# Kernel tuning notes

Hardware: AMD Instinct MI355X
Metric: run time of the kernel (lower is better)

The kernel has to match this reference:

```python
import jax, jax.numpy as jnp
import numpy as np

B, L, E, H, V = 64, 128, 512, 512, 32000  # batch, output_length, emb_dim, hidden, vocab


def setup_inputs() -> dict:
    key = jax.random.key(0)
    ks = jax.random.split(key, 9)
    g = lambda k, shape, sc=0.02: jax.random.normal(k, shape, jnp.float32) * sc
    return {
        "decoder_inputs": jax.random.randint(ks[0], (B, L), 0, V),
        "hidden": jax.random.normal(ks[1], (1, B, H), jnp.float32),  # size-only; zeroed in forward
        "encoder_outputs": jax.random.normal(ks[2], (B, L, H), jnp.float32),
        "emb_table": g(ks[3], (V, E)),
        "W_attn": g(ks[4], (L, 2 * H)),
        "b_attn": jnp.zeros((L,), jnp.float32),
        "W_ih": g(ks[5], (3 * H, E)),
        "W_hh": g(ks[6], (3 * H, H)),
        "b_ih": jnp.zeros((3 * H,), jnp.float32),
        "b_hh": jnp.zeros((3 * H,), jnp.float32),
        "W_out": g(ks[7], (V, H)),
        "b_out": jnp.zeros((V,), jnp.float32),
    }


def reference(decoder_inputs, hidden, encoder_outputs, emb_table, W_attn, b_attn,
              W_ih, W_hh, b_ih, b_hh, W_out, b_out):
    # teacher_force=True, train=True path; dropout = identity (eval semantics).
    T = L - 1  # output_length - 1 steps
    embedded = emb_table[decoder_inputs]                      # [B, L, E]
    h0 = jnp.zeros((B, H), embedded.dtype)                    # init_hidden(): hidden is zeroed
    # decode_input at step i is embedded[:, max(i-1, 0)] under teacher forcing
    prev_idx = jnp.maximum(jnp.arange(T) - 1, 0)
    dec_in_seq = jnp.transpose(embedded[:, prev_idx], (1, 0, 2))  # [T, B, E]
    x_seq = jnp.transpose(embedded[:, :T], (1, 0, 2))             # [T, B, E] GRU inputs
    tgt_seq = decoder_inputs[:, :T].T                             # [T, B]

    def step(carry, xs):
        h, loss = carry
        dec_in, x, tgt = xs
        attn_logits = jnp.concatenate([dec_in, h], axis=-1) @ W_attn.T + b_attn  # [B, L]
        aw = jax.nn.softmax(attn_logits, axis=-1)
        _ = jnp.einsum('bl,blh->bh', aw, encoder_outputs)  # attn_applied (computed, unused w/ teacher forcing)
        # single-step GRU cell (PyTorch gate order: r, z, n)
        gi = x @ W_ih.T + b_ih                                # [B, 3H]
        gh = h @ W_hh.T + b_hh
        ir, iz, inn = jnp.split(gi, 3, axis=-1)
        hr, hz, hn = jnp.split(gh, 3, axis=-1)
        r = jax.nn.sigmoid(ir + hr)
        z = jax.nn.sigmoid(iz + hz)
        n = jnp.tanh(inn + r * hn)
        h_new = (1.0 - z) * n + z * h
        logits = h_new @ W_out.T + b_out                      # [B, V]
        logp = jax.nn.log_softmax(logits, axis=-1)
        ce = -jnp.take_along_axis(logp, tgt[:, None], axis=1).mean()
        return (h_new, loss + ce), (aw, logits)

    (h_fin, loss), (attns, logits_all) = jax.lax.scan(
        step, (h0, jnp.asarray(0.0, jnp.float32)), (dec_in_seq, x_seq, tgt_seq))
    return loss, attns, h_fin[None], logits_all[-1]
```

## Files before the change

### kernel.cpp

```cpp
#include <hip/hip_runtime.h>
#include <math.h>

#define Bn 64
#define Lq 128
#define En 512
#define Hn 512
#define Vn 32000
#define Tn 127
#define MR 8128
#define MP 8192
#define NCB2 250
#define NBLK 36u

typedef __attribute__((ext_vector_type(8))) short short8v;
typedef __attribute__((ext_vector_type(4))) float f32x4;
typedef unsigned short ushort_t;

__device__ __forceinline__ ushort_t f2bf(float f) {
    unsigned u = __builtin_bit_cast(unsigned, f);
    u += 0x7fffu + ((u >> 16) & 1u);
    return (ushort_t)(u >> 16);
}
__device__ __forceinline__ float bf2f(ushort_t h) {
    return __builtin_bit_cast(float, ((unsigned)h) << 16);
}

constexpr size_t WS_BAR  = 0;
constexpr size_t WS_ZBH  = 64;
constexpr size_t WS_ZBL  = WS_ZBH + 65536;
constexpr size_t WS_WHHH = WS_ZBL + 65536;
constexpr size_t WS_WHHL = WS_WHHH + 1572864;
constexpr size_t WS_WAHH = WS_WHHL + 1572864;
constexpr size_t WS_WAHL = WS_WAHH + 131072;
constexpr size_t WS_HHI  = WS_WAHL + 131072;
constexpr size_t WS_HLO  = WS_HHI + 8388608;
constexpr size_t WS_U    = WS_HLO + 8388608;
constexpr size_t WS_GI   = WS_U;
constexpr size_t WS_GAX  = WS_U + 49938432;
constexpr size_t WS_WO16 = WS_U;
constexpr size_t WS_PM   = WS_U + 32768000;
constexpr size_t WS_PS   = WS_PM + 8192000;

__device__ __forceinline__ void grid_bar(unsigned* bar, unsigned tgt) {
    __syncthreads();
    if (threadIdx.x == 0) {
        __hip_atomic_fetch_add(bar, 1u, __ATOMIC_ACQ_REL, __HIP_MEMORY_SCOPE_AGENT);
        while (__hip_atomic_load(bar, __ATOMIC_RELAXED, __HIP_MEMORY_SCOPE_AGENT) < tgt) { }
        (void)__hip_atomic_load(bar, __ATOMIC_ACQUIRE, __HIP_MEMORY_SCOPE_AGENT);
    }
    __syncthreads();
}

__global__ __launch_bounds__(256) void setup_kernel(
    const float* __restrict__ Whh, const float* __restrict__ Wattn,
    ushort_t* __restrict__ zbh, ushort_t* __restrict__ zbl,
    ushort_t* __restrict__ whhh, ushort_t* __restrict__ whhl,
    ushort_t* __restrict__ wahh, ushort_t* __restrict__ wahl,
    ushort_t* __restrict__ Hhi, ushort_t* __restrict__ Hlo,
    unsigned* __restrict__ bar, float* __restrict__ out0)
{
    const int blk = blockIdx.x;
    const int t = threadIdx.x;
    if (blk < 256) {
        const int i = blk * 256 + t;
        if (i < Bn * Hn) { zbh[i] = 0; zbl[i] = 0; }
        else if (i < 2 * Bn * Hn) {
            const int j = i - Bn * Hn;
            Hhi[(size_t)MR * Hn + j] = 0;
            Hlo[(size_t)MR * Hn + j] = 0;
        }
        if (i == 0) { bar[0] = 0u; out0[0] = 0.0f; }
    } else {
        const int e = (blk - 256) * 256 + t;
        const int NW = 1536 * 512;
        if (e < NW) {
            const float wv = Whh[e]; const ushort_t h = f2bf(wv);
            whhh[e] = h; whhl[e] = f2bf(wv - bf2f(h));
        } else {
            const int e2 = e - NW;
            if (e2 < 128 * 512) {
                const int r = e2 >> 9, k = e2 & 511;
                const float wv = Wattn[r * 1024 + 512 + k]; const ushort_t h = f2bf(wv);
                wahh[e2] = h; wahl[e2] = f2bf(wv - bf2f(h));
            }
        }
    }
}

__global__ __launch_bounds__(256) void wout_cvt_kernel(
    const float* __restrict__ Wout, ushort_t* __restrict__ wo16)
{
    const size_t N = (size_t)Vn * Hn;
    for (size_t i = blockIdx.x * 256 + threadIdx.x; i < N; i += (size_t)gridDim.x * 256)
        wo16[i] = f2bf(Wout[i]);
}

#define PA 68
#define PW 132
__device__ void pre_tile(
    const int* __restrict__ idx, const float* __restrict__ emb,
    const float* __restrict__ Wb, int ldw, const float* __restrict__ bias,
    float* __restrict__ outp, int ldo, int ts, int cbase,
    float* As, float* Ws)
{
    const int t  = threadIdx.x;
    const int tr = t >> 4, tc = t & 15;

    float acc[4][8];
    #pragma unroll
    for (int q = 0; q < 4; q++)
        #pragma unroll
        for (int j = 0; j < 8; j++) acc[q][j] = 0.0f;

    const int ab = t & 63, kq = t >> 6;
    const int wc = t >> 1, wh = t & 1;

    for (int k0 = 0; k0 < 512; k0 += 32) {
        {
            const float* ap = emb + (size_t)idx[ab * Lq + ts] * En + k0 + kq * 8;
            const float4 v0 = *reinterpret_cast<const float4*>(ap);
            const float4 v1 = *reinterpret_cast<const float4*>(ap + 4);
            const int kk = kq * 8;
            As[(kk + 0) * PA + ab] = v0.x;  As[(kk + 1) * PA + ab] = v0.y;
            As[(kk + 2) * PA + ab] = v0.z;  As[(kk + 3) * PA + ab] = v0.w;
            As[(kk + 4) * PA + ab] = v1.x;  As[(kk + 5) * PA + ab] = v1.y;
            As[(kk + 6) * PA + ab] = v1.z;  As[(kk + 7) * PA + ab] = v1.w;
        }
        {
            const float* wp = Wb + (size_t)(cbase + wc) * ldw + k0 + wh * 16;
            const float4 w0 = reinterpret_cast<const float4*>(wp)[0];
            const float4 w1 = reinterpret_cast<const float4*>(wp)[1];
            const float4 w2 = reinterpret_cast<const float4*>(wp)[2];
            const float4 w3 = reinterpret_cast<const float4*>(wp)[3];
            const int kk = wh * 16;
            Ws[(kk + 0 ) * PW + wc] = w0.x; Ws[(kk + 1 ) * PW + wc] = w0.y;
            Ws[(kk + 2 ) * PW + wc] = w0.z; Ws[(kk + 3 ) * PW + wc] = w0.w;
            Ws[(kk + 4 ) * PW + wc] = w1.x; Ws[(kk + 5 ) * PW + wc] = w1.y;
            Ws[(kk + 6 ) * PW + wc] = w1.z; Ws[(kk + 7 ) * PW + wc] = w1.w;
            Ws[(kk + 8 ) * PW + wc] = w2.x; Ws[(kk + 9 ) * PW + wc] = w2.y;
            Ws[(kk + 10) * PW + wc] = w2.z; Ws[(kk + 11) * PW + wc] = w2.w;
            Ws[(kk + 12) * PW + wc] = w3.x; Ws[(kk + 13) * PW + wc] = w3.y;
            Ws[(kk + 14) * PW + wc] = w3.z; Ws[(kk + 15) * PW + wc] = w3.w;
        }
        __syncthreads();
        #pragma unroll 4
        for (int kk = 0; kk < 32; kk++) {
            const float4 av = *reinterpret_cast<const float4*>(&As[kk * PA + tr * 4]);
            const float4 w0 = *reinterpret_cast<const float4*>(&Ws[kk * PW + tc * 8]);
            const float4 w1 = *reinterpret_cast<const float4*>(&Ws[kk * PW + tc * 8 + 4]);
            const float a0 = av.x, a1 = av.y, a2 = av.z, a3 = av.w;
            const float w[8] = {w0.x, w0.y, w0.z, w0.w, w1.x, w1.y, w1.z, w1.w};
            #pragma unroll
            for (int j = 0; j < 8; j++) {
                acc[0][j] = fmaf(a0, w[j], acc[0][j]);
                acc[1][j] = fmaf(a1, w[j], acc[1][j]);
                acc[2][j] = fmaf(a2, w[j], acc[2][j]);
                acc[3][j] = fmaf(a3, w[j], acc[3][j]);
            }
        }
        __syncthreads();
    }

    #pragma unroll
    for (int q = 0; q < 4; q++) {
        const int row = tr * 4 + q;
        #pragma unroll
        for (int j = 0; j < 8; j++) {
            const int lc = tc * 8 + j;
            outp[((size_t)ts * 64 + row) * ldo + cbase + lc] = acc[q][j] + bias[cbase + lc];
        }
    }
}

__global__ __launch_bounds__(256) void pre_all_kernel(
    const int* __restrict__ idx, const float* __restrict__ emb,
    const float* __restrict__ Wih, const float* __restrict__ bih,
    const float* __restrict__ Wattn, const float* __restrict__ battn,
    float* __restrict__ Gi, float* __restrict__ Gax)
{
    __shared__ float As[32 * PA];
    __shared__ float Ws[32 * PW];
    const int blk = blockIdx.x;
    if (blk < Tn * 12) {
        pre_tile(idx, emb, Wih, 512, bih, Gi, 1536, blk / 12, (blk % 12) * 128, As, Ws);
    } else {
        pre_tile(idx, emb, Wattn, 1024, battn, Gax, 128, blk - Tn * 12, 0, As, Ws);
    }
}

__global__ __launch_bounds__(256) void recur_kernel(
    const ushort_t* __restrict__ zbh, const ushort_t* __restrict__ zbl,
    const ushort_t* __restrict__ whhh, const ushort_t* __restrict__ whhl,
    const ushort_t* __restrict__ wahh, const ushort_t* __restrict__ wahl,
    const float* __restrict__ Gi, const float* __restrict__ Gax,
    const float* __restrict__ b_hh,
    ushort_t* __restrict__ Hhi, ushort_t* __restrict__ Hlo,
    float* __restrict__ out_attn, float* __restrict__ out_hfin,
    unsigned* __restrict__ bar)
{
    __shared__ float lS[16][128];
    const int blk = blockIdx.x;
    const int t = threadIdx.x;
    const int w = t >> 6, l = t & 63, lr = l & 15, lg = l >> 4;

    if (blk < 32) {
        const int r0 = (blk >> 3) * 16;
        const int u0 = (blk & 7) * 64;
        const int c  = u0 + w * 16 + lr;
        const ushort_t* bh0 = whhh + (size_t)(c)        * Hn + lg * 8;
        const ushort_t* bh1 = whhh + (size_t)(512 + c)  * Hn + lg * 8;
        const ushort_t* bh2 = whhh + (size_t)(1024 + c) * Hn + lg * 8;
        const ushort_t* bl0 = whhl + (size_t)(c)        * Hn + lg * 8;
        const ushort_t* bl1 = whhl + (size_t)(512 + c)  * Hn + lg * 8;
        const ushort_t* bl2 = whhl + (size_t)(1024 + c) * Hn + lg * 8;
        const float bhr = b_hh[c], bhz = b_hh[512 + c], bhn = b_hh[1024 + c];

        for (int s = 0; s < Tn; s++) {
            const ushort_t* hh = (s == 0) ? zbh : (Hhi + (size_t)(s - 1) * (Bn * Hn));
            const ushort_t* hl = (s == 0) ? zbl : (Hlo + (size_t)(s - 1) * (Bn * Hn));
            const ushort_t* ah = hh + (size_t)(r0 + lr) * Hn + lg * 8;
            const ushort_t* al = hl + (size_t)(r0 + lr) * Hn + lg * 8;

            f32x4 a0 = {0.f,0.f,0.f,0.f}, a1 = {0.f,0.f,0.f,0.f}, a2 = {0.f,0.f,0.f,0.f};
            #pragma unroll 2
            for (int ks = 0; ks < 16; ks++) {
                const int k0 = ks * 32;
                const short8v xh  = *reinterpret_cast<const short8v*>(ah + k0);
                const short8v xlo = *reinterpret_cast<const short8v*>(al + k0);
                const short8v w0h = *reinterpret_cast<const short8v*>(bh0 + k0);
                const short8v w1h = *reinterpret_cast<const short8v*>(bh1 + k0);
                const short8v w2h = *reinterpret_cast<const short8v*>(bh2 + k0);
                const short8v w0l = *reinterpret_cast<const short8v*>(bl0 + k0);
                const short8v w1l = *reinterpret_cast<const short8v*>(bl1 + k0);
                const short8v w2l = *reinterpret_cast<const short8v*>(bl2 + k0);
                a0 = __builtin_amdgcn_mfma_f32_16x16x32_bf16(xh,  w0h, a0, 0, 0, 0);
                a0 = __builtin_amdgcn_mfma_f32_16x16x32_bf16(xlo, w0h, a0, 0, 0, 0);
                a0 = __builtin_amdgcn_mfma_f32_16x16x32_bf16(xh,  w0l, a0, 0, 0, 0);
                a1 = __builtin_amdgcn_mfma_f32_16x16x32_bf16(xh,  w1h, a1, 0, 0, 0);
                a1 = __builtin_amdgcn_mfma_f32_16x16x32_bf16(xlo, w1h, a1, 0, 0, 0);
                a1 = __builtin_amdgcn_mfma_f32_16x16x32_bf16(xh,  w1l, a1, 0, 0, 0);
                a2 = __builtin_amdgcn_mfma_f32_16x16x32_bf16(xh,  w2h, a2, 0, 0, 0);
                a2 = __builtin_amdgcn_mfma_f32_16x16x32_bf16(xlo, w2h, a2, 0, 0, 0);
                a2 = __builtin_amdgcn_mfma_f32_16x16x32_bf16(xh,  w2l, a2, 0, 0, 0);
            }
            #pragma unroll
            for (int i = 0; i < 4; i++) {
                const int grow = r0 + lg * 4 + i;
                const float* gib = Gi + ((size_t)s * Bn + grow) * 1536 + c;
                const float gir = gib[0], giz = gib[512], gin = gib[1024];
                const float ghr = a0[i] + bhr, ghz = a1[i] + bhz, ghn = a2[i] + bhn;
                const float rr = 1.0f / (1.0f + expf(-(gir + ghr)));
                const float zz = 1.0f / (1.0f + expf(-(giz + ghz)));
                const float nn = tanhf(gin + rr * ghn);
                const float ho = bf2f(hh[(size_t)grow * Hn + c]) + bf2f(hl[(size_t)grow * Hn + c]);
                const float hv = (1.0f - zz) * nn + zz * ho;
                const ushort_t hi = f2bf(hv);
                const size_t o = ((size_t)s * Bn + grow) * Hn + c;
                Hhi[o] = hi;
                Hlo[o] = f2bf(hv - bf2f(hi));
                if (s == Tn - 1) out_hfin[(size_t)grow * Hn + c] = hv;
            }
            if (s < Tn - 1) grid_bar(bar, NBLK * (unsigned)(s + 1));
        }
    } else {
        const int r0 = (blk - 32) * 16;
        const ushort_t* bh0 = wahh + (size_t)(w * 32 + lr)      * Hn + lg * 8;
        const ushort_t* bh1 = wahh + (size_t)(w * 32 + 16 + lr) * Hn + lg * 8;
        const ushort_t* bl0 = wahl + (size_t)(w * 32 + lr)      * Hn + lg * 8;
        const ushort_t* bl1 = wahl + (size_t)(w * 32 + 16 + lr) * Hn + lg * 8;

        for (int s = 0; s < Tn; s++) {
            const ushort_t* hh = (s == 0) ? zbh : (Hhi + (size_t)(s - 1) * (Bn * Hn));
            const ushort_t* hl = (s == 0) ? zbl : (Hlo + (size_t)(s - 1) * (Bn * Hn));
            const ushort_t* ah = hh + (size_t)(r0 + lr) * Hn + lg * 8;
            const ushort_t* al = hl + (size_t)(r0 + lr) * Hn + lg * 8;

            f32x4 c0a = {0.f,0.f,0.f,0.f}, c1a = {0.f,0.f,0.f,0.f};
            #pragma unroll 2
            for (int ks = 0; ks < 16; ks++) {
                const int k0 = ks * 32;
                const short8v xh  = *reinterpret_cast<const short8v*>(ah + k0);
                const short8v xlo = *reinterpret_cast<const short8v*>(al + k0);
                const short8v w0h = *reinterpret_cast<const short8v*>(bh0 + k0);
                const short8v w1h = *reinterpret_cast<const short8v*>(bh1 + k0);
                const short8v w0l = *reinterpret_cast<const short8v*>(bl0 + k0);
                const short8v w1l = *reinterpret_cast<const short8v*>(bl1 + k0);
                c0a = __builtin_amdgcn_mfma_f32_16x16x32_bf16(xh,  w0h, c0a, 0, 0, 0);
                c0a = __builtin_amdgcn_mfma_f32_16x16x32_bf16(xlo, w0h, c0a, 0, 0, 0);
                c0a = __builtin_amdgcn_mfma_f32_16x16x32_bf16(xh,  w0l, c0a, 0, 0, 0);
                c1a = __builtin_amdgcn_mfma_f32_16x16x32_bf16(xh,  w1h, c1a, 0, 0, 0);
                c1a = __builtin_amdgcn_mfma_f32_16x16x32_bf16(xlo, w1h, c1a, 0, 0, 0);
                c1a = __builtin_amdgcn_mfma_f32_16x16x32_bf16(xh,  w1l, c1a, 0, 0, 0);
            }
            const int jp = (s > 0) ? (s - 1) : 0;
            #pragma unroll
            for (int i = 0; i < 4; i++) {
                const int row = lg * 4 + i;
                const float* gax = Gax + ((size_t)jp * Bn + r0 + row) * Lq;
                lS[row][w * 32 + lr]      = c0a[i] + gax[w * 32 + lr];
                lS[row][w * 32 + 16 + lr] = c1a[i] + gax[w * 32 + 16 + lr];
            }
            __syncthreads();
            {
                const int row = t >> 4, l16 = t & 15;
                float m = -INFINITY;
                #pragma unroll
                for (int kx = 0; kx < 8; kx++) m = fmaxf(m, lS[row][l16 + kx * 16]);
                #pragma unroll
                for (int d = 1; d < 16; d <<= 1) m = fmaxf(m, __shfl_xor(m, d, 16));
                float sv = 0.0f;
                #pragma unroll
                for (int kx = 0; kx < 8; kx++) sv += expf(lS[row][l16 + kx * 16] - m);
                #pragma unroll
                for (int d = 1; d < 16; d <<= 1) sv += __shfl_xor(sv, d, 16);
                const float inv = 1.0f / sv;
                float* oa = out_attn + ((size_t)s * Bn + r0 + row) * Lq;
                #pragma unroll
                for (int kx = 0; kx < 8; kx++)
                    oa[l16 + kx * 16] = expf(lS[row][l16 + kx * 16] - m) * inv;
            }
            __syncthreads();
            if (s < Tn - 1) grid_bar(bar, NBLK * (unsigned)(s + 1));
        }
    }
}

__device__ __forceinline__ void stage16(const void* g, void* lds) {
    __builtin_amdgcn_global_load_lds(
        (const __attribute__((address_space(1))) unsigned int*)g,
        (__attribute__((address_space(3))) unsigned int*)lds, 16, 0, 0);
}

__global__ __launch_bounds__(256) void big_gemm2_kernel(
    const ushort_t* __restrict__ Hhi, const ushort_t* __restrict__ wo16,
    const float* __restrict__ bout,
    float* __restrict__ pm, float* __restrict__ ps,
    float* __restrict__ out_logits)
{
    __shared__ ushort_t lA[2][128 * 32];
    __shared__ ushort_t lB[2][128 * 32];
    __shared__ float sm[4][64];
    __shared__ float ssv[4][64];

    const int bid = blockIdx.x;
    const int cb = bid >> 6;
    const int rb = bid & 63;
    const int t = threadIdx.x;
    const int w = t >> 6, l = t & 63;
    const int lr = l & 15, lg = l >> 4;
    const int qr = (w >> 1) * 64;
    const int qc = (w & 1) * 64;
    const int r0 = rb * 128, c0 = cb * 128;

    const int srow = w * 16 + (l >> 2);
    const int skel = (((l & 3) ^ ((l >> 2) & 3))) * 8;
    const ushort_t* gA = Hhi  + (size_t)r0 * Hn;
    const ushort_t* gB = wo16 + (size_t)c0 * Hn;

    f32x4 acc[4][4];
    #pragma unroll
    for (int rt = 0; rt < 4; rt++)
        #pragma unroll
        for (int ct = 0; ct < 4; ct++)
            acc[rt][ct] = (f32x4){0.f, 0.f, 0.f, 0.f};

    #pragma unroll
    for (int j = 0; j < 2; j++) {
        const int row = j * 64 + srow;
        stage16(gA + (size_t)row * Hn + skel, &lA[0][(size_t)(j * 64 + w * 16) * 32]);
        stage16(gB + (size_t)row * Hn + skel, &lB[0][(size_t)(j * 64 + w * 16) * 32]);
    }

    int buf = 0;
    for (int ks = 0; ks < 16; ks++) {
        __syncthreads();
        if (ks < 15) {
            const int k0 = (ks + 1) * 32;
            #pragma unroll
            for (int j = 0; j < 2; j++) {
                const int row = j * 64 + srow;
                stage16(gA + (size_t)row * Hn + k0 + skel, &lA[buf ^ 1][(size_t)(j * 64 + w * 16) * 32]);
                stage16(gB + (size_t)row * Hn + k0 + skel, &lB[buf ^ 1][(size_t)(j * 64 + w * 16) * 32]);
            }
        }
        short8v a[4], b[4];
        #pragma unroll
        for (int rt = 0; rt < 4; rt++) {
            const int row = qr + rt * 16 + lr;
            a[rt] = *reinterpret_cast<const short8v*>(&lA[buf][row * 32 + ((lg ^ (row & 3)) * 8)]);
        }
        #pragma unroll
        for (int ct = 0; ct < 4; ct++) {
            const int row = qc + ct * 16 + lr;
            b[ct] = *reinterpret_cast<const short8v*>(&lB[buf][row * 32 + ((lg ^ (row & 3)) * 8)]);
        }
        #pragma unroll
        for (int rt = 0; rt < 4; rt++)
            #pragma unroll
            for (int ct = 0; ct < 4; ct++)
                acc[rt][ct] = __builtin_amdgcn_mfma_f32_16x16x32_bf16(a[rt], b[ct], acc[rt][ct], 0, 0, 0);
        buf ^= 1;
    }

    float biav[4];
    #pragma unroll
    for (int ct = 0; ct < 4; ct++) biav[ct] = bout[c0 + qc + ct * 16 + lr];

    #pragma unroll
    for (int rt = 0; rt < 4; rt++) {
        #pragma unroll
        for (int i = 0; i < 4; i++) {
            const int rowl_w = rt * 16 + lg * 4 + i;
            const int grow = r0 + qr + rowl_w;
            float v[4];
            #pragma unroll
            for (int ct = 0; ct < 4; ct++) v[ct] = acc[rt][ct][i] + biav[ct];
            if (grow >= MR - Bn && grow < MR) {
                const size_t ob = (size_t)(grow - (MR - Bn)) * Vn + c0 + qc + lr;
                out_logits[ob]      = v[0];
                out_logits[ob + 16] = v[1];
                out_logits[ob + 32] = v[2];
                out_logits[ob + 48] = v[3];
            }
            float m = fmaxf(fmaxf(v[0], v[1]), fmaxf(v[2], v[3]));
            #pragma unroll
            for (int d = 1; d < 16; d <<= 1) m = fmaxf(m, __shfl_xor(m, d));
            float sv = expf(v[0] - m) + expf(v[1] - m) + expf(v[2] - m) + expf(v[3] - m);
            #pragma unroll
            for (int d = 1; d < 16; d <<= 1) sv += __shfl_xor(sv, d);
            if (lr == 0) { sm[w][rowl_w] = m; ssv[w][rowl_w] = sv; }
        }
    }
    __syncthreads();
    if (t < 128) {
        const int half = t >> 6, rl = t & 63;
        const int wa = half * 2;
        float M = sm[wa][rl], S = ssv[wa][rl];
        const float m2 = sm[wa + 1][rl], s2 = ssv[wa + 1][rl];
        const float Mn = fmaxf(M, m2);
        S = S * expf(M - Mn) + s2 * expf(m2 - Mn);
        pm[(size_t)cb * MP + r0 + half * 64 + rl] = Mn;
        ps[(size_t)cb * MP + r0 + half * 64 + rl] = S;
    }
}

__global__ __launch_bounds__(256) void merge_loss_kernel(
    const float* __restrict__ pm, const float* __restrict__ ps,
    const ushort_t* __restrict__ Hhi, const ushort_t* __restrict__ Hlo,
    const int* __restrict__ idx, const float* __restrict__ Wout,
    const float* __restrict__ bout, float* __restrict__ out_loss)
{
    const int tt = blockIdx.x;
    const int t = threadIdx.x;
    const int b = t >> 2, q = t & 3;
    const int grow = tt * 64 + b;

    float M = -INFINITY, S = 0.0f;
    for (int p = q; p < NCB2; p += 4) {
        const float m2 = pm[(size_t)p * MP + grow], s2 = ps[(size_t)p * MP + grow];
        const float Mn = fmaxf(M, m2);
        S = S * expf(M - Mn) + s2 * expf(m2 - Mn);
        M = Mn;
    }
    #pragma unroll
    for (int d = 1; d < 4; d <<= 1) {
        const float m2 = __shfl_xor(M, d, 4);
        const float s2 = __shfl_xor(S, d, 4);
        const float Mn = fmaxf(M, m2);
        S = S * expf(M - Mn) + s2 * expf(m2 - Mn);
        M = Mn;
    }

    const int tgt = idx[b * Lq + tt];
    const size_t hb = (size_t)grow * Hn;
    const float* wr_ = Wout + (size_t)tgt * Hn;
    float dot = 0.0f;
    for (int k = q * 128; k < q * 128 + 128; k += 4) {
        #pragma unroll
        for (int j = 0; j < 4; j++) {
            const float hv = bf2f(Hhi[hb + k + j]) + bf2f(Hlo[hb + k + j]);
            dot = fmaf(hv, wr_[k + j], dot);
        }
    }
    #pragma unroll
    for (int d = 1; d < 4; d <<= 1) dot += __shfl_xor(dot, d, 4);

    __shared__ float ce[Bn];
    if (q == 0) ce[b] = -(dot + bout[tgt] - M - logf(S));
    __syncthreads();
    if (t == 0) {
        float s = 0.0f;
        for (int i = 0; i < Bn; i++) s += ce[i];
        atomicAdd(out_loss, s * (1.0f / Bn));
    }
}

extern "C" void kernel_launch(void* const* d_in, const int* in_sizes, int n_in,
                              void* d_out, int out_size, void* d_ws, size_t ws_size,
                              hipStream_t stream) {
    (void)in_sizes; (void)n_in; (void)out_size; (void)ws_size;
    const int*   idx    = (const int*)  d_in[0];
    const float* emb    = (const float*)d_in[3];
    const float* W_attn = (const float*)d_in[4];
    const float* b_attn = (const float*)d_in[5];
    const float* W_ih   = (const float*)d_in[6];
    const float* W_hh   = (const float*)d_in[7];
    const float* b_ih   = (const float*)d_in[8];
    const float* b_hh   = (const float*)d_in[9];
    const float* W_out  = (const float*)d_in[10];
    const float* b_out  = (const float*)d_in[11];

    float* out = (float*)d_out;
    float* out_attn   = out + 1;
    float* out_hfin   = out + 1 + (size_t)Tn * Bn * Lq;
    float* out_logits = out + 1 + (size_t)Tn * Bn * Lq + (size_t)Bn * Hn;

    char* W = (char*)d_ws;
    unsigned* bar   = (unsigned*)(W + WS_BAR);
    ushort_t* zbh   = (ushort_t*)(W + WS_ZBH);
    ushort_t* zbl   = (ushort_t*)(W + WS_ZBL);
    ushort_t* whhh  = (ushort_t*)(W + WS_WHHH);
    ushort_t* whhl  = (ushort_t*)(W + WS_WHHL);
    ushort_t* wahh  = (ushort_t*)(W + WS_WAHH);
    ushort_t* wahl  = (ushort_t*)(W + WS_WAHL);
    ushort_t* Hhi   = (ushort_t*)(W + WS_HHI);
    ushort_t* Hlo   = (ushort_t*)(W + WS_HLO);
    float*    Gi    = (float*)   (W + WS_GI);
    float*    Gax   = (float*)   (W + WS_GAX);
    ushort_t* wo16  = (ushort_t*)(W + WS_WO16);
    float*    pm    = (float*)   (W + WS_PM);
    float*    ps    = (float*)   (W + WS_PS);

    setup_kernel<<<dim3(3584), dim3(256), 0, stream>>>(
        W_hh, W_attn, zbh, zbl, whhh, whhl, wahh, wahl, Hhi, Hlo, bar, out);
    pre_all_kernel<<<dim3(Tn * 12 + Tn), dim3(256), 0, stream>>>(
        idx, emb, W_ih, b_ih, W_attn, b_attn, Gi, Gax);

    recur_kernel<<<dim3(NBLK), dim3(256), 0, stream>>>(
        zbh, zbl, whhh, whhl, wahh, wahl, Gi, Gax, b_hh,
        Hhi, Hlo, out_attn, out_hfin, bar);

    wout_cvt_kernel<<<dim3(2048), dim3(256), 0, stream>>>(W_out, wo16);
    big_gemm2_kernel<<<dim3(NCB2 * 64), dim3(256), 0, stream>>>(
        Hhi, wo16, b_out, pm, ps, out_logits);

    merge_loss_kernel<<<dim3(Tn), dim3(256), 0, stream>>>(
        pm, ps, Hhi, Hlo, idx, W_out, b_out, out);
}
```

Baseline: 3.510 ms.

## Replace grid barrier with per-block step flags and LDS-staged hidden state

The persistent recurrence kernel drops the global atomic grid barrier. The 32 GRU blocks now publish a per-block step counter, and every block waits only until all 32 flags reach the current step. At the start of each step, each block loads its 16-row hidden slice with cache-bypassing coherent loads into swizzled LDS, skips the zero matmul at step 0, and writes new hidden values with coherent stores. The attention blocks no longer take part in synchronization, which removes barrier round trips from the serial critical path, at the cost of relying on inline-asm memory ordering. The LDS swizzle pattern in the big output GEMM is also changed.

```diff
diff --git a/kernel.cpp b/kernel.cpp
--- a/kernel.cpp
+++ b/kernel.cpp
@@ -10,10 +10,10 @@
 #define MR 8128
 #define MP 8192
 #define NCB2 250
-#define NBLK 36u
 
 typedef __attribute__((ext_vector_type(8))) short short8v;
 typedef __attribute__((ext_vector_type(4))) float f32x4;
+typedef __attribute__((ext_vector_type(4))) unsigned int u32x4;
 typedef unsigned short ushort_t;
 
 __device__ __forceinline__ ushort_t f2bf(float f) {
@@ -25,51 +25,44 @@
     return __builtin_bit_cast(float, ((unsigned)h) << 16);
 }
 
-constexpr size_t WS_BAR  = 0;
-constexpr size_t WS_ZBH  = 64;
-constexpr size_t WS_ZBL  = WS_ZBH + 65536;
-constexpr size_t WS_WHHH = WS_ZBL + 65536;
-constexpr size_t WS_WHHL = WS_WHHH + 1572864;
-constexpr size_t WS_WAHH = WS_WHHL + 1572864;
-constexpr size_t WS_WAHL = WS_WAHH + 131072;
-constexpr size_t WS_HHI  = WS_WAHL + 131072;
-constexpr size_t WS_HLO  = WS_HHI + 8388608;
-constexpr size_t WS_U    = WS_HLO + 8388608;
-constexpr size_t WS_GI   = WS_U;
-constexpr size_t WS_GAX  = WS_U + 49938432;
-constexpr size_t WS_WO16 = WS_U;
-constexpr size_t WS_PM   = WS_U + 32768000;
-constexpr size_t WS_PS   = WS_PM + 8192000;
-
-__device__ __forceinline__ void grid_bar(unsigned* bar, unsigned tgt) {
-    __syncthreads();
-    if (threadIdx.x == 0) {
-        __hip_atomic_fetch_add(bar, 1u, __ATOMIC_ACQ_REL, __HIP_MEMORY_SCOPE_AGENT);
-        while (__hip_atomic_load(bar, __ATOMIC_RELAXED, __HIP_MEMORY_SCOPE_AGENT) < tgt) { }
-        (void)__hip_atomic_load(bar, __ATOMIC_ACQUIRE, __HIP_MEMORY_SCOPE_AGENT);
-    }
-    __syncthreads();
-}
+__device__ __forceinline__ u32x4 ld_coh_x4(const void* p) {
+    u32x4 r;
+    asm volatile("global_load_dwordx4 %0, %1, off sc0 sc1" : "=&v"(r) : "v"(p));
+    return r;
+}
+__device__ __forceinline__ void st_coh_u16(void* p, unsigned v) {
+    asm volatile("global_store_short %0, %1, off sc0 sc1" :: "v"(p), "v"(v) : "memory");
+}
+
+constexpr size_t WS_FLAGS = 0;
+constexpr size_t WS_WHHH  = 128;
+constexpr size_t WS_WHHL  = WS_WHHH + 1572864;
+constexpr size_t WS_WAHH  = WS_WHHL + 1572864;
+constexpr size_t WS_WAHL  = WS_WAHH + 131072;
+constexpr size_t WS_HHI   = WS_WAHL + 131072;
+constexpr size_t WS_HLO   = WS_HHI + 8388608;
+constexpr size_t WS_U     = WS_HLO + 8388608;
+constexpr size_t WS_GI    = WS_U;
+constexpr size_t WS_GAX   = WS_U + 49938432;
+constexpr size_t WS_WO16  = WS_U;
+constexpr size_t WS_PM    = WS_U + 32768000;
+constexpr size_t WS_PS    = WS_PM + 8192000;
 
 __global__ __launch_bounds__(256) void setup_kernel(
     const float* __restrict__ Whh, const float* __restrict__ Wattn,
-    ushort_t* __restrict__ zbh, ushort_t* __restrict__ zbl,
     ushort_t* __restrict__ whhh, ushort_t* __restrict__ whhl,
     ushort_t* __restrict__ wahh, ushort_t* __restrict__ wahl,
     ushort_t* __restrict__ Hhi, ushort_t* __restrict__ Hlo,
-    unsigned* __restrict__ bar, float* __restrict__ out0)
+    unsigned* __restrict__ flags, float* __restrict__ out0)
 {
     const int blk = blockIdx.x;
     const int t = threadIdx.x;
     if (blk < 256) {
         const int i = blk * 256 + t;
-        if (i < Bn * Hn) { zbh[i] = 0; zbl[i] = 0; }
-        else if (i < 2 * Bn * Hn) {
-            const int j = i - Bn * Hn;
-            Hhi[(size_t)MR * Hn + j] = 0;
-            Hlo[(size_t)MR * Hn + j] = 0;
-        }
-        if (i == 0) { bar[0] = 0u; out0[0] = 0.0f; }
+        if (i < Bn * Hn) Hhi[(size_t)MR * Hn + i] = 0;
+        else if (i < 2 * Bn * Hn) Hlo[(size_t)MR * Hn + (i - Bn * Hn)] = 0;
+        if (blk == 0 && t < 32) flags[t] = 0u;
+        if (blk == 0 && t == 32) out0[0] = 0.0f;
     } else {
         const int e = (blk - 256) * 256 + t;
         const int NW = 1536 * 512;
@@ -189,108 +182,155 @@
 }
 
 __global__ __launch_bounds__(256) void recur_kernel(
-    const ushort_t* __restrict__ zbh, const ushort_t* __restrict__ zbl,
     const ushort_t* __restrict__ whhh, const ushort_t* __restrict__ whhl,
     const ushort_t* __restrict__ wahh, const ushort_t* __restrict__ wahl,
     const float* __restrict__ Gi, const float* __restrict__ Gax,
     const float* __restrict__ b_hh,
     ushort_t* __restrict__ Hhi, ushort_t* __restrict__ Hlo,
     float* __restrict__ out_attn, float* __restrict__ out_hfin,
-    unsigned* __restrict__ bar)
-{
+    unsigned* __restrict__ flags)
+{
+    __shared__ ushort_t lA[16384];
     __shared__ float lS[16][128];
+
     const int blk = blockIdx.x;
     const int t = threadIdx.x;
     const int w = t >> 6, l = t & 63, lr = l & 15, lg = l >> 4;
-
-    if (blk < 32) {
-        const int r0 = (blk >> 3) * 16;
-        const int u0 = (blk & 7) * 64;
-        const int c  = u0 + w * 16 + lr;
-        const ushort_t* bh0 = whhh + (size_t)(c)        * Hn + lg * 8;
-        const ushort_t* bh1 = whhh + (size_t)(512 + c)  * Hn + lg * 8;
-        const ushort_t* bh2 = whhh + (size_t)(1024 + c) * Hn + lg * 8;
-        const ushort_t* bl0 = whhl + (size_t)(c)        * Hn + lg * 8;
-        const ushort_t* bl1 = whhl + (size_t)(512 + c)  * Hn + lg * 8;
-        const ushort_t* bl2 = whhl + (size_t)(1024 + c) * Hn + lg * 8;
-        const float bhr = b_hh[c], bhz = b_hh[512 + c], bhn = b_hh[1024 + c];
-
-        for (int s = 0; s < Tn; s++) {
-            const ushort_t* hh = (s == 0) ? zbh : (Hhi + (size_t)(s - 1) * (Bn * Hn));
-            const ushort_t* hl = (s == 0) ? zbl : (Hlo + (size_t)(s - 1) * (Bn * Hn));
-            const ushort_t* ah = hh + (size_t)(r0 + lr) * Hn + lg * 8;
-            const ushort_t* al = hl + (size_t)(r0 + lr) * Hn + lg * 8;
-
+    const bool isg = (blk < 32);
+    const int r0 = isg ? ((blk >> 3) * 16) : ((blk - 32) * 16);
+    const int u0 = isg ? ((blk & 7) * 64) : 0;
+    const int c  = u0 + w * 16 + lr;
+
+    const ushort_t *pw0h, *pw1h, *pw2h, *pw0l, *pw1l, *pw2l;
+    float bhr = 0.f, bhz = 0.f, bhn = 0.f;
+    if (isg) {
+        pw0h = whhh + (size_t)(c)        * Hn + lg * 8;
+        pw1h = whhh + (size_t)(512 + c)  * Hn + lg * 8;
+        pw2h = whhh + (size_t)(1024 + c) * Hn + lg * 8;
+        pw0l = whhl + (size_t)(c)        * Hn + lg * 8;
+        pw1l = whhl + (size_t)(512 + c)  * Hn + lg * 8;
+        pw2l = whhl + (size_t)(1024 + c) * Hn + lg * 8;
+        bhr = b_hh[c]; bhz = b_hh[512 + c]; bhn = b_hh[1024 + c];
+    } else {
+        pw0h = wahh + (size_t)(w * 32 + lr)      * Hn + lg * 8;
+        pw1h = wahh + (size_t)(w * 32 + 16 + lr) * Hn + lg * 8;
+        pw0l = wahl + (size_t)(w * 32 + lr)      * Hn + lg * 8;
+        pw1l = wahl + (size_t)(w * 32 + 16 + lr) * Hn + lg * 8;
+        pw2h = pw0h; pw2l = pw0l;
+    }
+
+    const int erow = t >> 4;
+    const int ecol = (t & 15) * 32;
+    const int swzw = (erow & 7) << 4;
+    const int b0 = erow * 1024 + ecol * 2;
+
+    for (int s = 0; s < Tn; s++) {
+        if (s > 0) {
+            unsigned f = 0xFFFFFFFFu;
+            if (l < 32) f = __hip_atomic_load(&flags[l], __ATOMIC_RELAXED, __HIP_MEMORY_SCOPE_AGENT);
+            while (__any((int)(f < (unsigned)s))) {
+                if (l < 32) f = __hip_atomic_load(&flags[l], __ATOMIC_RELAXED, __HIP_MEMORY_SCOPE_AGENT);
+            }
+            asm volatile("" ::: "memory");
+            const size_t gb = ((size_t)(s - 1) * Bn + r0 + erow) * Hn + ecol;
+            const u32x4 h0 = ld_coh_x4(Hhi + gb);
+            const u32x4 h1 = ld_coh_x4(Hhi + gb + 8);
+            const u32x4 h2 = ld_coh_x4(Hhi + gb + 16);
+            const u32x4 h3 = ld_coh_x4(Hhi + gb + 24);
+            const u32x4 o0 = ld_coh_x4(Hlo + gb);
+            const u32x4 o1 = ld_coh_x4(Hlo + gb + 8);
+            const u32x4 o2 = ld_coh_x4(Hlo + gb + 16);
+            const u32x4 o3 = ld_coh_x4(Hlo + gb + 24);
+            asm volatile("s_waitcnt vmcnt(0)" ::: "memory");
+            char* dst = (char*)lA;
+            *(u32x4*)(dst + ((b0     ) ^ swzw)) = h0;
+            *(u32x4*)(dst + ((b0 + 16) ^ swzw)) = h1;
+            *(u32x4*)(dst + ((b0 + 32) ^ swzw)) = h2;
+            *(u32x4*)(dst + ((b0 + 48) ^ swzw)) = h3;
+            *(u32x4*)(dst + 16384 + ((b0     ) ^ swzw)) = o0;
+            *(u32x4*)(dst + 16384 + ((b0 + 16) ^ swzw)) = o1;
+            *(u32x4*)(dst + 16384 + ((b0 + 32) ^ swzw)) = o2;
+            *(u32x4*)(dst + 16384 + ((b0 + 48) ^ swzw)) = o3;
+            __syncthreads();
+        }
+
+        if (isg) {
             f32x4 a0 = {0.f,0.f,0.f,0.f}, a1 = {0.f,0.f,0.f,0.f}, a2 = {0.f,0.f,0.f,0.f};
-            #pragma unroll 2
-            for (int ks = 0; ks < 16; ks++) {
-                const int k0 = ks * 32;
-                const short8v xh  = *reinterpret_cast<const short8v*>(ah + k0);
-                const short8v xlo = *reinterpret_cast<const short8v*>(al + k0);
-                const short8v w0h = *reinterpret_cast<const short8v*>(bh0 + k0);
-                const short8v w1h = *reinterpret_cast<const short8v*>(bh1 + k0);
-                const short8v w2h = *reinterpret_cast<const short8v*>(bh2 + k0);
-                const short8v w0l = *reinterpret_cast<const short8v*>(bl0 + k0);
-                const short8v w1l = *reinterpret_cast<const short8v*>(bl1 + k0);
-                const short8v w2l = *reinterpret_cast<const short8v*>(bl2 + k0);
-                a0 = __builtin_amdgcn_mfma_f32_16x16x32_bf16(xh,  w0h, a0, 0, 0, 0);
-                a0 = __builtin_amdgcn_mfma_f32_16x16x32_bf16(xlo, w0h, a0, 0, 0, 0);
-                a0 = __builtin_amdgcn_mfma_f32_16x16x32_bf16(xh,  w0l, a0, 0, 0, 0);
-                a1 = __builtin_amdgcn_mfma_f32_16x16x32_bf16(xh,  w1h, a1, 0, 0, 0);
-                a1 = __builtin_amdgcn_mfma_f32_16x16x32_bf16(xlo, w1h, a1, 0, 0, 0);
-                a1 = __builtin_amdgcn_mfma_f32_16x16x32_bf16(xh,  w1l, a1, 0, 0, 0);
-                a2 = __builtin_amdgcn_mfma_f32_16x16x32_bf16(xh,  w2h, a2, 0, 0, 0);
-                a2 = __builtin_amdgcn_mfma_f32_16x16x32_bf16(xlo, w2h, a2, 0, 0, 0);
-                a2 = __builtin_amdgcn_mfma_f32_16x16x32_bf16(xh,  w2l, a2, 0, 0, 0);
+            if (s > 0) {
+                const int swzr = (lr & 7) << 4;
+                #pragma unroll 2
+                for (int ks = 0; ks < 16; ks++) {
+                    const int ab = (lr * 1024 + ks * 64 + lg * 16) ^ swzr;
+                    const short8v xh = *(const short8v*)((char*)lA + ab);
+                    const short8v xl = *(const short8v*)((char*)lA + 16384 + ab);
+                    const int ko = ks * 32;
+                    const short8v w0h = *(const short8v*)(pw0h + ko);
+                    const short8v w1h = *(const short8v*)(pw1h + ko);
+                    const short8v w2h = *(const short8v*)(pw2h + ko);
+                    const short8v w0l = *(const short8v*)(pw0l + ko);
+                    const short8v w1l = *(const short8v*)(pw1l + ko);
+                    const short8v w2l = *(const short8v*)(pw2l + ko);
+                    a0 = __builtin_amdgcn_mfma_f32_16x16x32_bf16(xh, w0h, a0, 0, 0, 0);
+                    a0 = __builtin_amdgcn_mfma_f32_16x16x32_bf16(xl, w0h, a0, 0, 0, 0);
+                    a0 = __builtin_amdgcn_mfma_f32_16x16x32_bf16(xh, w0l, a0, 0, 0, 0);
+                    a1 = __builtin_amdgcn_mfma_f32_16x16x32_bf16(xh, w1h, a1, 0, 0, 0);
+                    a1 = __builtin_amdgcn_mfma_f32_16x16x32_bf16(xl, w1h, a1, 0, 0, 0);
+                    a1 = __builtin_amdgcn_mfma_f32_16x16x32_bf16(xh, w1l, a1, 0, 0, 0);
+                    a2 = __builtin_amdgcn_mfma_f32_16x16x32_bf16(xh, w2h, a2, 0, 0, 0);
+                    a2 = __builtin_amdgcn_mfma_f32_16x16x32_bf16(xl, w2h, a2, 0, 0, 0);
+                    a2 = __builtin_amdgcn_mfma_f32_16x16x32_bf16(xh, w2l, a2, 0, 0, 0);
+                }
             }
             #pragma unroll
             for (int i = 0; i < 4; i++) {
-                const int grow = r0 + lg * 4 + i;
+                const int row16 = lg * 4 + i;
+                const int grow = r0 + row16;
                 const float* gib = Gi + ((size_t)s * Bn + grow) * 1536 + c;
                 const float gir = gib[0], giz = gib[512], gin = gib[1024];
                 const float ghr = a0[i] + bhr, ghz = a1[i] + bhz, ghn = a2[i] + bhn;
                 const float rr = 1.0f / (1.0f + expf(-(gir + ghr)));
                 const float zz = 1.0f / (1.0f + expf(-(giz + ghz)));
                 const float nn = tanhf(gin + rr * ghn);
-                const float ho = bf2f(hh[(size_t)grow * Hn + c]) + bf2f(hl[(size_t)grow * Hn + c]);
+                float ho = 0.0f;
+                if (s > 0) {
+                    const int hb = (row16 * 1024 + c * 2) ^ ((row16 & 7) << 4);
+                    ho = bf2f(*(const ushort_t*)((char*)lA + hb))
+                       + bf2f(*(const ushort_t*)((char*)lA + 16384 + hb));
+                }
                 const float hv = (1.0f - zz) * nn + zz * ho;
                 const ushort_t hi = f2bf(hv);
+                const ushort_t lo = f2bf(hv - bf2f(hi));
                 const size_t o = ((size_t)s * Bn + grow) * Hn + c;
-                Hhi[o] = hi;
-                Hlo[o] = f2bf(hv - bf2f(hi));
+                st_coh_u16(Hhi + o, (unsigned)hi);
+                st_coh_u16(Hlo + o, (unsigned)lo);
                 if (s == Tn - 1) out_hfin[(size_t)grow * Hn + c] = hv;
             }
-            if (s < Tn - 1) grid_bar(bar, NBLK * (unsigned)(s + 1));
-        }
-    } else {
-        const int r0 = (blk - 32) * 16;
-        const ushort_t* bh0 = wahh + (size_t)(w * 32 + lr)      * Hn + lg * 8;
-        const ushort_t* bh1 = wahh + (size_t)(w * 32 + 16 + lr) * Hn + lg * 8;
-        const ushort_t* bl0 = wahl + (size_t)(w * 32 + lr)      * Hn + lg * 8;
-        const ushort_t* bl1 = wahl + (size_t)(w * 32 + 16 + lr) * Hn + lg * 8;
-
-        for (int s = 0; s < Tn; s++) {
-            const ushort_t* hh = (s == 0) ? zbh : (Hhi + (size_t)(s - 1) * (Bn * Hn));
-            const ushort_t* hl = (s == 0) ? zbl : (Hlo + (size_t)(s - 1) * (Bn * Hn));
-            const ushort_t* ah = hh + (size_t)(r0 + lr) * Hn + lg * 8;
-            const ushort_t* al = hl + (size_t)(r0 + lr) * Hn + lg * 8;
-
+            asm volatile("s_waitcnt vmcnt(0)" ::: "memory");
+            __syncthreads();
+            if (t == 0)
+                __hip_atomic_store(&flags[blk], (unsigned)(s + 1),
+                                   __ATOMIC_RELAXED, __HIP_MEMORY_SCOPE_AGENT);
+        } else {
             f32x4 c0a = {0.f,0.f,0.f,0.f}, c1a = {0.f,0.f,0.f,0.f};
-            #pragma unroll 2
-            for (int ks = 0; ks < 16; ks++) {
-                const int k0 = ks * 32;
-                const short8v xh  = *reinterpret_cast<const short8v*>(ah + k0);
-                const short8v xlo = *reinterpret_cast<const short8v*>(al + k0);
-                const short8v w0h = *reinterpret_cast<const short8v*>(bh0 + k0);
-                const short8v w1h = *reinterpret_cast<const short8v*>(bh1 + k0);
-                const short8v w0l = *reinterpret_cast<const short8v*>(bl0 + k0);
-                const short8v w1l = *reinterpret_cast<const short8v*>(bl1 + k0);
-                c0a = __builtin_amdgcn_mfma_f32_16x16x32_bf16(xh,  w0h, c0a, 0, 0, 0);
-                c0a = __builtin_amdgcn_mfma_f32_16x16x32_bf16(xlo, w0h, c0a, 0, 0, 0);
-                c0a = __builtin_amdgcn_mfma_f32_16x16x32_bf16(xh,  w0l, c0a, 0, 0, 0);
-                c1a = __builtin_amdgcn_mfma_f32_16x16x32_bf16(xh,  w1h, c1a, 0, 0, 0);
-                c1a = __builtin_amdgcn_mfma_f32_16x16x32_bf16(xlo, w1h, c1a, 0, 0, 0);
-                c1a = __builtin_amdgcn_mfma_f32_16x16x32_bf16(xh,  w1l, c1a, 0, 0, 0);
+            if (s > 0) {
+                const int swzr = (lr & 7) << 4;
+                #pragma unroll 2
+                for (int ks = 0; ks < 16; ks++) {
+                    const int ab = (lr * 1024 + ks * 64 + lg * 16) ^ swzr;
+                    const short8v xh = *(const short8v*)((char*)lA + ab);
+                    const short8v xl = *(const short8v*)((char*)lA + 16384 + ab);
+                    const int ko = ks * 32;
+                    const short8v w0h = *(const short8v*)(pw0h + ko);
+                    const short8v w1h = *(const short8v*)(pw1h + ko);
+                    const short8v w0l = *(const short8v*)(pw0l + ko);
+                    const short8v w1l = *(const short8v*)(pw1l + ko);
+                    c0a = __builtin_amdgcn_mfma_f32_16x16x32_bf16(xh, w0h, c0a, 0, 0, 0);
+                    c0a = __builtin_amdgcn_mfma_f32_16x16x32_bf16(xl, w0h, c0a, 0, 0, 0);
+                    c0a = __builtin_amdgcn_mfma_f32_16x16x32_bf16(xh, w0l, c0a, 0, 0, 0);
+                    c1a = __builtin_amdgcn_mfma_f32_16x16x32_bf16(xh, w1h, c1a, 0, 0, 0);
+                    c1a = __builtin_amdgcn_mfma_f32_16x16x32_bf16(xl, w1h, c1a, 0, 0, 0);
+                    c1a = __builtin_amdgcn_mfma_f32_16x16x32_bf16(xh, w1l, c1a, 0, 0, 0);
+                }
             }
             const int jp = (s > 0) ? (s - 1) : 0;
             #pragma unroll
@@ -320,7 +360,6 @@
                     oa[l16 + kx * 16] = expf(lS[row][l16 + kx * 16] - m) * inv;
             }
             __syncthreads();
-            if (s < Tn - 1) grid_bar(bar, NBLK * (unsigned)(s + 1));
         }
     }
 }
@@ -353,7 +392,7 @@
     const int r0 = rb * 128, c0 = cb * 128;
 
     const int srow = w * 16 + (l >> 2);
-    const int skel = (((l & 3) ^ ((l >> 2) & 3))) * 8;
+    const int skel = (((l & 3) ^ ((l >> 3) & 3))) * 8;
     const ushort_t* gA = Hhi  + (size_t)r0 * Hn;
     const ushort_t* gB = wo16 + (size_t)c0 * Hn;
 
@@ -387,12 +426,12 @@
         #pragma unroll
         for (int rt = 0; rt < 4; rt++) {
             const int row = qr + rt * 16 + lr;
-            a[rt] = *reinterpret_cast<const short8v*>(&lA[buf][row * 32 + ((lg ^ (row & 3)) * 8)]);
+            a[rt] = *reinterpret_cast<const short8v*>(&lA[buf][row * 32 + ((lg ^ ((row >> 1) & 3)) * 8)]);
         }
         #pragma unroll
         for (int ct = 0; ct < 4; ct++) {
             const int row = qc + ct * 16 + lr;
-            b[ct] = *reinterpret_cast<const short8v*>(&lB[buf][row * 32 + ((lg ^ (row & 3)) * 8)]);
+            b[ct] = *reinterpret_cast<const short8v*>(&lB[buf][row * 32 + ((lg ^ ((row >> 1) & 3)) * 8)]);
         }
         #pragma unroll
         for (int rt = 0; rt < 4; rt++)
@@ -516,9 +555,7 @@
     float* out_logits = out + 1 + (size_t)Tn * Bn * Lq + (size_t)Bn * Hn;
 
     char* W = (char*)d_ws;
-    unsigned* bar   = (unsigned*)(W + WS_BAR);
-    ushort_t* zbh   = (ushort_t*)(W + WS_ZBH);
-    ushort_t* zbl   = (ushort_t*)(W + WS_ZBL);
+    unsigned* flags = (unsigned*)(W + WS_FLAGS);
     ushort_t* whhh  = (ushort_t*)(W + WS_WHHH);
     ushort_t* whhl  = (ushort_t*)(W + WS_WHHL);
     ushort_t* wahh  = (ushort_t*)(W + WS_WAHH);
@@ -532,13 +569,13 @@
     float*    ps    = (float*)   (W + WS_PS);
 
     setup_kernel<<<dim3(3584), dim3(256), 0, stream>>>(
-        W_hh, W_attn, zbh, zbl, whhh, whhl, wahh, wahl, Hhi, Hlo, bar, out);
+        W_hh, W_attn, whhh, whhl, wahh, wahl, Hhi, Hlo, flags, out);
     pre_all_kernel<<<dim3(Tn * 12 + Tn), dim3(256), 0, stream>>>(
         idx, emb, W_ih, b_ih, W_attn, b_attn, Gi, Gax);
 
-    recur_kernel<<<dim3(NBLK), dim3(256), 0, stream>>>(
-        zbh, zbl, whhh, whhl, wahh, wahl, Gi, Gax, b_hh,
-        Hhi, Hlo, out_attn, out_hfin, bar);
+    recur_kernel<<<dim3(36), dim3(256), 0, stream>>>(
+        whhh, whhl, wahh, wahl, Gi, Gax, b_hh,
+        Hhi, Hlo, out_attn, out_hfin, flags);
 
     wout_cvt_kernel<<<dim3(2048), dim3(256), 0, stream>>>(W_out, wo16);
     big_gemm2_kernel<<<dim3(NCB2 * 64), dim3(256), 0, stream>>>(
```

New measurement: 3.060 ms. 1.15x faster.
